# Performance work log

Measured on AMD Instinct MI355X. Metric: run time of the kernel, lower is better.

The kernel has to match this reference:

```python
import jax, jax.numpy as jnp
import numpy as np

N_NODES = 50000
N_EDGES = 1600000
IN_FEAT = 128
HIDDEN = 128
CLASSES = 2


def gin_conv(x, src, dst, W, b, n_nodes):
    # GINConv (eps=0): h_i = mlp(x_i + sum_{j in N(i)} x_j)
    agg = jax.ops.segment_sum(x[src], dst, num_segments=n_nodes)  # [N, F]
    h = x + agg
    return h @ W + b


def setup_inputs() -> dict:
    key = jax.random.key(0)
    ks = jax.random.split(key, 8)
    x = jax.random.normal(ks[0], (N_NODES, IN_FEAT), dtype=jnp.float32)
    edge_index = jax.random.randint(ks[1], (2, N_EDGES), 0, N_NODES, dtype=jnp.int64)
    def lin(k, fan_in, fan_out):
        kw, kb = jax.random.split(k)
        bound = 1.0 / np.sqrt(fan_in)
        W = jax.random.uniform(kw, (fan_in, fan_out), jnp.float32, -bound, bound)
        b = jax.random.uniform(kb, (fan_out,), jnp.float32, -bound, bound)
        return W, b
    W1, b1 = lin(ks[2], IN_FEAT, HIDDEN)
    W2, b2 = lin(ks[3], HIDDEN, HIDDEN)
    W3, b3 = lin(ks[4], HIDDEN, CLASSES)
    return {"x": x, "edge_index": edge_index, "W1": W1, "b1": b1,
            "W2": W2, "b2": b2, "W3": W3, "b3": b3}


def reference(x, edge_index, W1, b1, W2, b2, W3, b3):
    src, dst = edge_index[0], edge_index[1]
    n = x.shape[0]
    h = jax.nn.relu(gin_conv(x, src, dst, W1, b1, n))
    h = jax.nn.relu(gin_conv(h, src, dst, W2, b2, n))
    return gin_conv(h, src, dst, W3, b3, n)
```

## Files before the change

### kernel.cpp

```cpp
#include <hip/hip_runtime.h>

#define NNODES 50000
#define NEDGES 1600000
#define F 128

#define NB 128
#define BSH 391
#define BCAP 13312
#define EPT 10

typedef __attribute__((ext_vector_type(8))) short bf16x8;
typedef __attribute__((ext_vector_type(4))) float f32x4;

__device__ inline unsigned short f2bf(float f) {
    union { float f; unsigned u; } v; v.f = f;
    unsigned r = v.u + 0x7FFF + ((v.u >> 16) & 1);
    return (unsigned short)(r >> 16);
}
__device__ inline float2 up2(ushort2 h) {
    union { unsigned u; float f; } a, b;
    a.u = ((unsigned)h.x) << 16; b.u = ((unsigned)h.y) << 16;
    return make_float2(a.f, b.f);
}

__global__ __launch_bounds__(256) void cvt_bf16(const float4* __restrict__ in,
                                                ushort4* __restrict__ out, int n4) {
    int i = blockIdx.x * blockDim.x + threadIdx.x;
    int stride = gridDim.x * blockDim.x;
    for (; i < n4; i += stride) {
        float4 v = in[i];
        ushort4 o;
        o.x = f2bf(v.x); o.y = f2bf(v.y); o.z = f2bf(v.z); o.w = f2bf(v.w);
        out[i] = o;
    }
}

__global__ __launch_bounds__(256) void wprep2(const float* __restrict__ W1,
                                              const float* __restrict__ W2,
                                              unsigned short* __restrict__ Wf1,
                                              unsigned short* __restrict__ Wf2,
                                              int* __restrict__ gcnt) {
    int id = blockIdx.x * 256 + threadIdx.x;
    if (blockIdx.x == 0 && threadIdx.x < NB) gcnt[threadIdx.x] = 0;
    const float* W = (id < 2048) ? W1 : W2;
    unsigned short* Wf = (id < 2048) ? Wf1 : Wf2;
    id &= 2047;
    const int l = id & 63, nn = (id >> 6) & 7, s = id >> 9;
    const int c = nn * 16 + (l & 15);
    const int k0 = s * 32 + (l >> 4) * 8;
    ushort4 lo, hi;
    lo.x = f2bf(W[(k0 + 0) * F + c]); lo.y = f2bf(W[(k0 + 1) * F + c]);
    lo.z = f2bf(W[(k0 + 2) * F + c]); lo.w = f2bf(W[(k0 + 3) * F + c]);
    hi.x = f2bf(W[(k0 + 4) * F + c]); hi.y = f2bf(W[(k0 + 5) * F + c]);
    hi.z = f2bf(W[(k0 + 6) * F + c]); hi.w = f2bf(W[(k0 + 7) * F + c]);
    ushort4* p = (ushort4*)(Wf + (size_t)id * 8);
    p[0] = lo; p[1] = hi;
}

__global__ __launch_bounds__(256) void bucketA(const int* __restrict__ src,
                                               const int* __restrict__ dst,
                                               unsigned* __restrict__ E1,
                                               int* __restrict__ gcnt) {
    __shared__ unsigned hist[4][NB];
    __shared__ unsigned start[4][NB];
    const int t = threadIdx.x, w = t >> 6;
    for (int i = t; i < 4 * NB; i += 256) ((unsigned*)hist)[i] = 0;
    __syncthreads();
    const int base = blockIdx.x * (256 * EPT);
    unsigned rec[EPT]; int bkt[EPT];
#pragma unroll
    for (int k = 0; k < EPT; ++k) {
        const int i = base + k * 256 + t;
        const int s = src[i], d = dst[i];
        const int b = d / BSH;
        rec[k] = ((unsigned)s << 9) | (unsigned)(d - b * BSH);
        bkt[k] = b;
        atomicAdd(&hist[w][b], 1u);
    }
    __syncthreads();
    if (t < NB) {
        const unsigned h0 = hist[0][t], h1 = hist[1][t], h2 = hist[2][t], h3 = hist[3][t];
        const unsigned tot = h0 + h1 + h2 + h3;
        const unsigned g = tot ? (unsigned)atomicAdd(&gcnt[t], (int)tot) : 0u;
        start[0][t] = g;
        start[1][t] = g + h0;
        start[2][t] = g + h0 + h1;
        start[3][t] = g + h0 + h1 + h2;
        hist[0][t] = 0; hist[1][t] = 0; hist[2][t] = 0; hist[3][t] = 0;
    }
    __syncthreads();
#pragma unroll
    for (int k = 0; k < EPT; ++k) {
        const int b = bkt[k];
        const unsigned p = start[w][b] + atomicAdd(&hist[w][b], 1u);
        if (p < BCAP) E1[(size_t)b * BCAP + p] = rec[k];
    }
}

__global__ __launch_bounds__(256) void bucketB(const unsigned* __restrict__ E1,
                                               const int* __restrict__ gcnt,
                                               int* __restrict__ off,
                                               unsigned short* __restrict__ ssrc) {
    __shared__ int cnt[BSH];
    __shared__ int cur[BSH];
    __shared__ int wtot[4];
    __shared__ int bst[NB];
    const int b = blockIdx.x, t = threadIdx.x;
    if (t < 64) {
        const int a0 = gcnt[t * 2], a1 = gcnt[t * 2 + 1];
        const int s = a0 + a1;
        int inc = s;
#pragma unroll
        for (int o = 1; o <= 32; o <<= 1) {
            int u = __shfl_up(inc, o);
            if (t >= o) inc += u;
        }
        bst[t * 2] = inc - s;
        bst[t * 2 + 1] = inc - s + a0;
    }
    for (int i = t; i < BSH; i += 256) cnt[i] = 0;
    __syncthreads();
    const int ne = min(gcnt[b], BCAP);
    const int ebase = bst[b];
    const unsigned* E = E1 + (size_t)b * BCAP;
    for (int i = t; i < ne; i += 256) atomicAdd(&cnt[E[i] & 511], 1);
    __syncthreads();
    const int i0 = t * 2, i1 = t * 2 + 1;
    const int a0 = (i0 < BSH) ? cnt[i0] : 0;
    const int a1 = (i1 < BSH) ? cnt[i1] : 0;
    const int s = a0 + a1;
    int inc = s;
    const int lane = t & 63, w = t >> 6;
#pragma unroll
    for (int o = 1; o <= 32; o <<= 1) {
        int u = __shfl_up(inc, o);
        if (lane >= o) inc += u;
    }
    if (lane == 63) wtot[w] = inc;
    __syncthreads();
    int woff = 0;
    for (int k = 0; k < w; ++k) woff += wtot[k];
    const int excl = woff + inc - s;
    if (i0 < BSH) {
        cur[i0] = excl;
        const int n = b * BSH + i0;
        if (n < NNODES) off[n] = ebase + excl;
    }
    if (i1 < BSH) {
        cur[i1] = excl + a0;
        const int n = b * BSH + i1;
        if (n < NNODES) off[n] = ebase + excl + a0;
    }
    if (b == NB - 1 && t == 0) off[NNODES] = NEDGES;
    __syncthreads();
    for (int i = t; i < ne; i += 256) {
        const unsigned rec = E[i];
        const int r = atomicAdd(&cur[rec & 511], 1);
        ssrc[ebase + r] = (unsigned short)(rec >> 9);
    }
}

__global__ __launch_bounds__(256) void agg_bf16(const ushort2* __restrict__ h,
                                                const int* __restrict__ off,
                                                const unsigned short* __restrict__ ssrc,
                                                ushort2* __restrict__ S, int n) {
    const int wid = (blockIdx.x * blockDim.x + threadIdx.x) >> 6;
    const int lane = threadIdx.x & 63;
    if (wid >= n) return;
    const int e0 = off[wid], e1 = off[wid + 1];
    float2 acc = up2(h[(size_t)wid * 64 + lane]);
    for (int base = e0; base < e1; base += 64) {
        const int cnt = min(64, e1 - base);
        const int myidx = (base + lane < e1) ? (int)ssrc[base + lane] : 0;
        int i = 0;
        for (; i + 8 <= cnt; i += 8) {
            const int s0 = __shfl(myidx, i + 0), s1 = __shfl(myidx, i + 1);
            const int s2 = __shfl(myidx, i + 2), s3 = __shfl(myidx, i + 3);
            const int s4 = __shfl(myidx, i + 4), s5 = __shfl(myidx, i + 5);
            const int s6 = __shfl(myidx, i + 6), s7 = __shfl(myidx, i + 7);
            const float2 v0 = up2(h[(size_t)s0 * 64 + lane]);
            const float2 v1 = up2(h[(size_t)s1 * 64 + lane]);
            const float2 v2 = up2(h[(size_t)s2 * 64 + lane]);
            const float2 v3 = up2(h[(size_t)s3 * 64 + lane]);
            const float2 v4 = up2(h[(size_t)s4 * 64 + lane]);
            const float2 v5 = up2(h[(size_t)s5 * 64 + lane]);
            const float2 v6 = up2(h[(size_t)s6 * 64 + lane]);
            const float2 v7 = up2(h[(size_t)s7 * 64 + lane]);
            acc.x += ((v0.x + v1.x) + (v2.x + v3.x)) + ((v4.x + v5.x) + (v6.x + v7.x));
            acc.y += ((v0.y + v1.y) + (v2.y + v3.y)) + ((v4.y + v5.y) + (v6.y + v7.y));
        }
        for (; i < cnt; ++i) {
            const int s = __shfl(myidx, i);
            const float2 v = up2(h[(size_t)s * 64 + lane]);
            acc.x += v.x;
            acc.y += v.y;
        }
    }
    ushort2 o;
    o.x = f2bf(acc.x); o.y = f2bf(acc.y);
    S[(size_t)wid * 64 + lane] = o;
}

__global__ __launch_bounds__(256) void mlp_mfma(const unsigned short* __restrict__ Sb,
                                                const unsigned short* __restrict__ Wfrag,
                                                const float* __restrict__ bias,
                                                unsigned short* __restrict__ Hb,
                                                int n, int relu) {
    const int wave = threadIdx.x >> 6, lane = threadIdx.x & 63;
    const int base = blockIdx.x * 64 + wave * 16;
    const int r16 = lane & 15, hi = lane >> 4;
    int arow = base + r16;
    if (arow >= n) arow = n - 1;
    const unsigned short* Arow = Sb + (size_t)arow * F;

    f32x4 acc[8];
#pragma unroll
    for (int i = 0; i < 8; ++i) acc[i] = (f32x4){0.f, 0.f, 0.f, 0.f};

#pragma unroll
    for (int s = 0; s < 4; ++s) {
        const bf16x8 a = *(const bf16x8*)(Arow + s * 32 + hi * 8);
#pragma unroll
        for (int nn = 0; nn < 8; ++nn) {
            const bf16x8 b = *(const bf16x8*)(Wfrag + ((size_t)(s * 8 + nn) * 64 + lane) * 8);
            acc[nn] = __builtin_amdgcn_mfma_f32_16x16x32_bf16(a, b, acc[nn], 0, 0, 0);
        }
    }

#pragma unroll
    for (int nn = 0; nn < 8; ++nn) {
        const int col = nn * 16 + r16;
        const float bv = bias[col];
#pragma unroll
        for (int r = 0; r < 4; ++r) {
            const int row = base + hi * 4 + r;
            if (row < n) {
                float v = acc[nn][r] + bv;
                if (relu) v = fmaxf(v, 0.f);
                Hb[(size_t)row * F + col] = f2bf(v);
            }
        }
    }
}

__global__ __launch_bounds__(256) void head_t(const ushort2* __restrict__ Hb,
                                              const float4* __restrict__ W3,
                                              float2* __restrict__ y, int n) {
    const int wid = (blockIdx.x * blockDim.x + threadIdx.x) >> 6;
    const int lane = threadIdx.x & 63;
    if (wid >= n) return;
    const float2 h = up2(Hb[(size_t)wid * 64 + lane]);
    const float4 w = W3[lane];
    float a0 = h.x * w.x + h.y * w.z;
    float a1 = h.x * w.y + h.y * w.w;
#pragma unroll
    for (int o = 32; o; o >>= 1) {
        a0 += __shfl_xor(a0, o);
        a1 += __shfl_xor(a1, o);
    }
    if (lane == 0) y[wid] = make_float2(a0, a1);
}

__global__ __launch_bounds__(256) void agg3(const float2* __restrict__ y,
                                            const int* __restrict__ off,
                                            const unsigned short* __restrict__ ssrc,
                                            const float* __restrict__ b3,
                                            float2* __restrict__ out, int n) {
    const int i = blockIdx.x * blockDim.x + threadIdx.x;
    if (i >= n) return;
    float2 acc = y[i];
    const int e1 = off[i + 1];
    for (int e = off[i]; e < e1; ++e) {
        const float2 v = y[ssrc[e]];
        acc.x += v.x;
        acc.y += v.y;
    }
    out[i] = make_float2(acc.x + b3[0], acc.y + b3[1]);
}

extern "C" void kernel_launch(void* const* d_in, const int* in_sizes, int n_in,
                              void* d_out, int out_size, void* d_ws, size_t ws_size,
                              hipStream_t stream) {
    const float* x  = (const float*)d_in[0];
    const int* ei   = (const int*)d_in[1];
    const int* src  = ei;
    const int* dst  = ei + NEDGES;
    const float* W1 = (const float*)d_in[2];
    const float* b1 = (const float*)d_in[3];
    const float* W2 = (const float*)d_in[4];
    const float* b2 = (const float*)d_in[5];
    const float* W3 = (const float*)d_in[6];
    const float* b3 = (const float*)d_in[7];
    float* out = (float*)d_out;

    char* ws = (char*)d_ws;
    const size_t featB = (size_t)NNODES * F * 2;
    unsigned short* xb = (unsigned short*)ws;
    unsigned short* Sb = (unsigned short*)(ws + featB);
    unsigned short* Hb = (unsigned short*)(ws + 2 * featB);
    char* p = ws + 3 * featB;
    float* y3 = (float*)p;                 p += (size_t)NNODES * 2 * 4 + 256;
    unsigned short* Wf1 = (unsigned short*)p; p += 2048 * 8 * 2;
    unsigned short* Wf2 = (unsigned short*)p; p += 2048 * 8 * 2;
    unsigned* E1 = (unsigned*)p;           p += (size_t)NB * BCAP * 4;
    int* gcnt = (int*)p;                   p += NB * 4 + 256;
    int* off = (int*)p;                    p += (size_t)(NNODES + 1) * 4 + 256;
    unsigned short* ssrc = (unsigned short*)p;

    cvt_bf16<<<1024, 256, 0, stream>>>((const float4*)x, (ushort4*)xb, NNODES * F / 4);
    wprep2<<<16, 256, 0, stream>>>(W1, W2, Wf1, Wf2, gcnt);

    bucketA<<<NEDGES / (256 * EPT), 256, 0, stream>>>(src, dst, E1, gcnt);
    bucketB<<<NB, 256, 0, stream>>>(E1, gcnt, off, ssrc);

    const int aggBlocks = (NNODES + 3) / 4;
    const int mlpBlocks = (NNODES + 63) / 64;

    agg_bf16<<<aggBlocks, 256, 0, stream>>>((const ushort2*)xb, off, ssrc, (ushort2*)Sb, NNODES);
    mlp_mfma<<<mlpBlocks, 256, 0, stream>>>(Sb, Wf1, b1, Hb, NNODES, 1);

    agg_bf16<<<aggBlocks, 256, 0, stream>>>((const ushort2*)Hb, off, ssrc, (ushort2*)Sb, NNODES);
    mlp_mfma<<<mlpBlocks, 256, 0, stream>>>(Sb, Wf2, b2, xb, NNODES, 1);

    head_t<<<aggBlocks, 256, 0, stream>>>((const ushort2*)xb, (const float4*)W3, (float2*)y3, NNODES);
    agg3<<<(NNODES + 255) / 256, 256, 0, stream>>>((const float2*)y3, off, ssrc, b3, (float2*)out, NNODES);
}
```

Measured before the change: 291.3 us.

## Fuse neighbor aggregation with MFMA MLP via LDS staging, reuse bucket ranks

Aggregation and the bf16 MFMA linear layer now run in one kernel. Each wave gathers 16 nodes, with two half-waves each taking an edge and loading ushort4 per lane. The aggregated rows go into swizzled shared memory and are fed straight to MFMA, so the intermediate S buffer no longer makes a round trip through global memory and one launch per layer is dropped. The bucket sort also keeps the rank returned by the first histogram atomic, removing the second atomic pass. The trade-off is fewer, heavier blocks: each wave handles 16 nodes serially, which lowers parallelism for latency hiding during the gather.

```diff
diff --git a/kernel.cpp b/kernel.cpp
--- a/kernel.cpp
+++ b/kernel.cpp
@@ -17,10 +17,10 @@
     unsigned r = v.u + 0x7FFF + ((v.u >> 16) & 1);
     return (unsigned short)(r >> 16);
 }
-__device__ inline float2 up2(ushort2 h) {
-    union { unsigned u; float f; } a, b;
-    a.u = ((unsigned)h.x) << 16; b.u = ((unsigned)h.y) << 16;
-    return make_float2(a.f, b.f);
+__device__ inline float b2f(unsigned short h) {
+    union { unsigned u; float f; } a;
+    a.u = ((unsigned)h) << 16;
+    return a.f;
 }
 
 __global__ __launch_bounds__(256) void cvt_bf16(const float4* __restrict__ in,
@@ -67,7 +67,7 @@
     for (int i = t; i < 4 * NB; i += 256) ((unsigned*)hist)[i] = 0;
     __syncthreads();
     const int base = blockIdx.x * (256 * EPT);
-    unsigned rec[EPT]; int bkt[EPT];
+    unsigned rec[EPT]; int bkt[EPT]; unsigned rnk[EPT];
 #pragma unroll
     for (int k = 0; k < EPT; ++k) {
         const int i = base + k * 256 + t;
@@ -75,7 +75,7 @@
         const int b = d / BSH;
         rec[k] = ((unsigned)s << 9) | (unsigned)(d - b * BSH);
         bkt[k] = b;
-        atomicAdd(&hist[w][b], 1u);
+        rnk[k] = atomicAdd(&hist[w][b], 1u);
     }
     __syncthreads();
     if (t < NB) {
@@ -86,14 +86,12 @@
         start[1][t] = g + h0;
         start[2][t] = g + h0 + h1;
         start[3][t] = g + h0 + h1 + h2;
-        hist[0][t] = 0; hist[1][t] = 0; hist[2][t] = 0; hist[3][t] = 0;
     }
     __syncthreads();
 #pragma unroll
     for (int k = 0; k < EPT; ++k) {
-        const int b = bkt[k];
-        const unsigned p = start[w][b] + atomicAdd(&hist[w][b], 1u);
-        if (p < BCAP) E1[(size_t)b * BCAP + p] = rec[k];
+        const unsigned p = start[w][bkt[k]] + rnk[k];
+        if (p < BCAP) E1[(size_t)bkt[k] * BCAP + p] = rec[k];
     }
 }
 
@@ -160,99 +158,103 @@
     }
 }
 
-__global__ __launch_bounds__(256) void agg_bf16(const ushort2* __restrict__ h,
-                                                const int* __restrict__ off,
-                                                const unsigned short* __restrict__ ssrc,
-                                                ushort2* __restrict__ S, int n) {
-    const int wid = (blockIdx.x * blockDim.x + threadIdx.x) >> 6;
-    const int lane = threadIdx.x & 63;
-    if (wid >= n) return;
-    const int e0 = off[wid], e1 = off[wid + 1];
-    float2 acc = up2(h[(size_t)wid * 64 + lane]);
-    for (int base = e0; base < e1; base += 64) {
-        const int cnt = min(64, e1 - base);
-        const int myidx = (base + lane < e1) ? (int)ssrc[base + lane] : 0;
-        int i = 0;
-        for (; i + 8 <= cnt; i += 8) {
-            const int s0 = __shfl(myidx, i + 0), s1 = __shfl(myidx, i + 1);
-            const int s2 = __shfl(myidx, i + 2), s3 = __shfl(myidx, i + 3);
-            const int s4 = __shfl(myidx, i + 4), s5 = __shfl(myidx, i + 5);
-            const int s6 = __shfl(myidx, i + 6), s7 = __shfl(myidx, i + 7);
-            const float2 v0 = up2(h[(size_t)s0 * 64 + lane]);
-            const float2 v1 = up2(h[(size_t)s1 * 64 + lane]);
-            const float2 v2 = up2(h[(size_t)s2 * 64 + lane]);
-            const float2 v3 = up2(h[(size_t)s3 * 64 + lane]);
-            const float2 v4 = up2(h[(size_t)s4 * 64 + lane]);
-            const float2 v5 = up2(h[(size_t)s5 * 64 + lane]);
-            const float2 v6 = up2(h[(size_t)s6 * 64 + lane]);
-            const float2 v7 = up2(h[(size_t)s7 * 64 + lane]);
-            acc.x += ((v0.x + v1.x) + (v2.x + v3.x)) + ((v4.x + v5.x) + (v6.x + v7.x));
-            acc.y += ((v0.y + v1.y) + (v2.y + v3.y)) + ((v4.y + v5.y) + (v6.y + v7.y));
-        }
-        for (; i < cnt; ++i) {
-            const int s = __shfl(myidx, i);
-            const float2 v = up2(h[(size_t)s * 64 + lane]);
-            acc.x += v.x;
-            acc.y += v.y;
-        }
-    }
-    ushort2 o;
-    o.x = f2bf(acc.x); o.y = f2bf(acc.y);
-    S[(size_t)wid * 64 + lane] = o;
-}
-
-__global__ __launch_bounds__(256) void mlp_mfma(const unsigned short* __restrict__ Sb,
-                                                const unsigned short* __restrict__ Wfrag,
-                                                const float* __restrict__ bias,
-                                                unsigned short* __restrict__ Hb,
-                                                int n, int relu) {
-    const int wave = threadIdx.x >> 6, lane = threadIdx.x & 63;
-    const int base = blockIdx.x * 64 + wave * 16;
+__global__ __launch_bounds__(256) void agg_mlp(const unsigned short* __restrict__ h,
+                                               const int* __restrict__ off,
+                                               const unsigned short* __restrict__ ssrc,
+                                               const unsigned short* __restrict__ Wfrag,
+                                               const float* __restrict__ bias,
+                                               unsigned short* __restrict__ out,
+                                               int n, int relu) {
+    __shared__ unsigned short Sl[4][16][128];
+    const int w = threadIdx.x >> 6, lane = threadIdx.x & 63;
+    const int nbase = blockIdx.x * 64 + w * 16;
+    const int half = lane >> 5, l32 = lane & 31;
+
+    for (int m = 0; m < 16; ++m) {
+        const int node = nbase + m;
+        float a0 = 0.f, a1 = 0.f, a2 = 0.f, a3 = 0.f;
+        if (node < n) {
+            const int e0 = off[node], e1 = off[node + 1];
+            if (half == 0) {
+                const ushort4 sv = *(const ushort4*)(h + (size_t)node * F + l32 * 4);
+                a0 = b2f(sv.x); a1 = b2f(sv.y); a2 = b2f(sv.z); a3 = b2f(sv.w);
+            }
+            for (int eb = e0; eb < e1; eb += 64) {
+                const int cnt = min(64, e1 - eb);
+                const int myidx = (eb + lane < e1) ? (int)ssrc[eb + lane] : 0;
+                int j = 0;
+                for (; j + 8 <= cnt; j += 8) {
+                    const int s0 = __shfl(myidx, j + 0 + half);
+                    const int s1 = __shfl(myidx, j + 2 + half);
+                    const int s2 = __shfl(myidx, j + 4 + half);
+                    const int s3 = __shfl(myidx, j + 6 + half);
+                    const ushort4 v0 = *(const ushort4*)(h + (size_t)s0 * F + l32 * 4);
+                    const ushort4 v1 = *(const ushort4*)(h + (size_t)s1 * F + l32 * 4);
+                    const ushort4 v2 = *(const ushort4*)(h + (size_t)s2 * F + l32 * 4);
+                    const ushort4 v3 = *(const ushort4*)(h + (size_t)s3 * F + l32 * 4);
+                    a0 += (b2f(v0.x) + b2f(v1.x)) + (b2f(v2.x) + b2f(v3.x));
+                    a1 += (b2f(v0.y) + b2f(v1.y)) + (b2f(v2.y) + b2f(v3.y));
+                    a2 += (b2f(v0.z) + b2f(v1.z)) + (b2f(v2.z) + b2f(v3.z));
+                    a3 += (b2f(v0.w) + b2f(v1.w)) + (b2f(v2.w) + b2f(v3.w));
+                }
+                for (; j < cnt; j += 2) {
+                    const int s = __shfl(myidx, min(j + half, cnt - 1));
+                    if (j + half < cnt) {
+                        const ushort4 v = *(const ushort4*)(h + (size_t)s * F + l32 * 4);
+                        a0 += b2f(v.x); a1 += b2f(v.y); a2 += b2f(v.z); a3 += b2f(v.w);
+                    }
+                }
+            }
+        }
+        a0 += __shfl_xor(a0, 32); a1 += __shfl_xor(a1, 32);
+        a2 += __shfl_xor(a2, 32); a3 += __shfl_xor(a3, 32);
+        if (half == 0) {
+            ushort4 wbv;
+            wbv.x = f2bf(a0); wbv.y = f2bf(a1); wbv.z = f2bf(a2); wbv.w = f2bf(a3);
+            *(ushort4*)(&Sl[w][m][(l32 * 4) ^ ((m & 7) << 3)]) = wbv;
+        }
+    }
+
     const int r16 = lane & 15, hi = lane >> 4;
-    int arow = base + r16;
-    if (arow >= n) arow = n - 1;
-    const unsigned short* Arow = Sb + (size_t)arow * F;
-
     f32x4 acc[8];
 #pragma unroll
     for (int i = 0; i < 8; ++i) acc[i] = (f32x4){0.f, 0.f, 0.f, 0.f};
-
 #pragma unroll
     for (int s = 0; s < 4; ++s) {
-        const bf16x8 a = *(const bf16x8*)(Arow + s * 32 + hi * 8);
+        const bf16x8 a = *(const bf16x8*)(&Sl[w][r16][(s * 32 + hi * 8) ^ ((r16 & 7) << 3)]);
 #pragma unroll
         for (int nn = 0; nn < 8; ++nn) {
             const bf16x8 b = *(const bf16x8*)(Wfrag + ((size_t)(s * 8 + nn) * 64 + lane) * 8);
             acc[nn] = __builtin_amdgcn_mfma_f32_16x16x32_bf16(a, b, acc[nn], 0, 0, 0);
         }
     }
-
 #pragma unroll
     for (int nn = 0; nn < 8; ++nn) {
         const int col = nn * 16 + r16;
         const float bv = bias[col];
 #pragma unroll
         for (int r = 0; r < 4; ++r) {
-            const int row = base + hi * 4 + r;
+            const int row = nbase + hi * 4 + r;
             if (row < n) {
                 float v = acc[nn][r] + bv;
                 if (relu) v = fmaxf(v, 0.f);
-                Hb[(size_t)row * F + col] = f2bf(v);
+                out[(size_t)row * F + col] = f2bf(v);
             }
         }
     }
 }
 
-__global__ __launch_bounds__(256) void head_t(const ushort2* __restrict__ Hb,
+__global__ __launch_bounds__(256) void head_t(const unsigned short* __restrict__ Hb,
                                               const float4* __restrict__ W3,
                                               float2* __restrict__ y, int n) {
     const int wid = (blockIdx.x * blockDim.x + threadIdx.x) >> 6;
     const int lane = threadIdx.x & 63;
     if (wid >= n) return;
-    const float2 h = up2(Hb[(size_t)wid * 64 + lane]);
+    const unsigned short* hp = Hb + (size_t)wid * F + lane * 2;
+    const float hx = b2f(hp[0]), hy = b2f(hp[1]);
     const float4 w = W3[lane];
-    float a0 = h.x * w.x + h.y * w.z;
-    float a1 = h.x * w.y + h.y * w.w;
+    float a0 = hx * w.x + hy * w.z;
+    float a1 = hx * w.y + hy * w.w;
 #pragma unroll
     for (int o = 32; o; o >>= 1) {
         a0 += __shfl_xor(a0, o);
@@ -296,9 +298,8 @@
     char* ws = (char*)d_ws;
     const size_t featB = (size_t)NNODES * F * 2;
     unsigned short* xb = (unsigned short*)ws;
-    unsigned short* Sb = (unsigned short*)(ws + featB);
-    unsigned short* Hb = (unsigned short*)(ws + 2 * featB);
-    char* p = ws + 3 * featB;
+    unsigned short* Hb = (unsigned short*)(ws + featB);
+    char* p = ws + 2 * featB;
     float* y3 = (float*)p;                 p += (size_t)NNODES * 2 * 4 + 256;
     unsigned short* Wf1 = (unsigned short*)p; p += 2048 * 8 * 2;
     unsigned short* Wf2 = (unsigned short*)p; p += 2048 * 8 * 2;
@@ -313,15 +314,11 @@
     bucketA<<<NEDGES / (256 * EPT), 256, 0, stream>>>(src, dst, E1, gcnt);
     bucketB<<<NB, 256, 0, stream>>>(E1, gcnt, off, ssrc);
 
-    const int aggBlocks = (NNODES + 3) / 4;
-    const int mlpBlocks = (NNODES + 63) / 64;
-
-    agg_bf16<<<aggBlocks, 256, 0, stream>>>((const ushort2*)xb, off, ssrc, (ushort2*)Sb, NNODES);
-    mlp_mfma<<<mlpBlocks, 256, 0, stream>>>(Sb, Wf1, b1, Hb, NNODES, 1);
-
-    agg_bf16<<<aggBlocks, 256, 0, stream>>>((const ushort2*)Hb, off, ssrc, (ushort2*)Sb, NNODES);
-    mlp_mfma<<<mlpBlocks, 256, 0, stream>>>(Sb, Wf2, b2, xb, NNODES, 1);
-
-    head_t<<<aggBlocks, 256, 0, stream>>>((const ushort2*)xb, (const float4*)W3, (float2*)y3, NNODES);
+    const int fusedBlocks = (NNODES + 63) / 64;
+
+    agg_mlp<<<fusedBlocks, 256, 0, stream>>>(xb, off, ssrc, Wf1, b1, Hb, NNODES, 1);
+    agg_mlp<<<fusedBlocks, 256, 0, stream>>>(Hb, off, ssrc, Wf2, b2, xb, NNODES, 1);
+
+    head_t<<<(NNODES + 3) / 4, 256, 0, stream>>>(xb, (const float4*)W3, (float2*)y3, NNODES);
     agg3<<<(NNODES + 255) / 256, 256, 0, stream>>>((const float2*)y3, off, ssrc, b3, (float2*)out, NNODES);
 }
```

New measurement: 315.7 us. 1.08x slower.
